# Optimization experiments

Hardware: AMD Instinct MI355X
Metric: run time of the kernel (lower is better)

The kernel has to match this reference:

```python
import jax, jax.numpy as jnp
import numpy as np

N, E = 50000, 800000
DIN, DOUT, DIM, K = 64, 64, 3, 8
EPS_GMM = 1e-15
BN_EPS = 1e-5
ALPHA = 0.01


def setup_inputs() -> dict:
    key = jax.random.key(0)
    ks = jax.random.split(key, 10)
    x = jax.random.normal(ks[0], (N, DIN), dtype=jnp.float32)
    edge_idx = jax.random.randint(ks[1], (2, E), 0, N, dtype=jnp.int64)
    edge_attr = jax.random.uniform(ks[2], (E, DIM), dtype=jnp.float32)
    # GMMConv params (PyG: g maps in -> K*out, lin is root weight, plus bias)
    W_g = jax.random.normal(ks[3], (DIN, K * DOUT), dtype=jnp.float32) * (1.0 / np.sqrt(DIN))
    mu = jax.random.normal(ks[4], (K, DIM), dtype=jnp.float32)
    sigma = jnp.ones((K, DIM), dtype=jnp.float32) + 0.1 * jax.random.normal(ks[5], (K, DIM), dtype=jnp.float32)
    W_root = jax.random.normal(ks[6], (DIN, DOUT), dtype=jnp.float32) * (1.0 / np.sqrt(DIN))
    bias = jnp.zeros((DOUT,), dtype=jnp.float32)
    gamma = jnp.ones((DOUT,), dtype=jnp.float32)
    beta = jnp.zeros((DOUT,), dtype=jnp.float32)
    return {"x": x, "edge_idx": edge_idx, "edge_attr": edge_attr,
            "W_g": W_g, "mu": mu, "sigma": sigma, "W_root": W_root,
            "bias": bias, "gamma": gamma, "beta": beta}


def reference(x, edge_idx, edge_attr, W_g, mu, sigma, W_root, bias, gamma, beta):
    src, dst = edge_idx[0], edge_idx[1]
    # Gaussian mixture edge weights: [E, K]
    diff = edge_attr[:, None, :] - mu[None, :, :]              # [E, K, DIM]
    gauss = jnp.exp((-0.5 * diff * diff / (EPS_GMM + sigma[None] ** 2)).sum(-1))  # [E, K]
    # Transform node features once: [N, K, DOUT]
    x_trans = (x @ W_g).reshape(N, K, DOUT)
    # Per-edge message: weighted sum over kernels of gathered source features
    msg = jnp.einsum('ekm,ek->em', x_trans[src], gauss)        # [E, DOUT]
    # Mean-aggregate to destination nodes
    agg = jax.ops.segment_sum(msg, dst, num_segments=N)        # [N, DOUT]
    cnt = jax.ops.segment_sum(jnp.ones((E,), dtype=x.dtype), dst, num_segments=N)
    agg = agg / jnp.maximum(cnt, 1.0)[:, None]
    # Root weight + bias
    out = agg + x @ W_root + bias
    # BatchNorm1d (training mode: batch stats, biased variance)
    m = out.mean(axis=0)
    v = ((out - m) ** 2).mean(axis=0)
    out = gamma * (out - m) * jax.lax.rsqrt(v + BN_EPS) + beta
    # LeakyReLU
    return jnp.where(out > 0, out, ALPHA * out)
```

## Files before the change

kernel.cpp:

```cpp
#include <hip/hip_runtime.h>
#include <hip/hip_bf16.h>

#define N_NODES 50000
#define N_EDGES 800000

__device__ __forceinline__ void store_val(float* p, float v) { *p = v; }
__device__ __forceinline__ void store_val(__hip_bfloat16* p, float v) { *p = __float2bfloat16(v); }
__device__ __forceinline__ float load_val(const float* p) { return *p; }
__device__ __forceinline__ float load_val(const __hip_bfloat16* p) { return __bfloat162float(*p); }

__global__ void prep_c1_kernel(const float* __restrict__ sigma, float* __restrict__ c1) {
    int i = threadIdx.x;
    if (i < 24) {
        float s = sigma[i];
        c1[i] = -0.5f / (s * s + 1e-15f);
    }
}

template <typename T>
__global__ void gemm_xt_kernel(const float* __restrict__ x, const float* __restrict__ Wg,
                               T* __restrict__ xt) {
    __shared__ float xs[16][64];
    const int tid = threadIdx.x;
    const int row0 = blockIdx.x << 4;
    for (int i = tid; i < 1024; i += 256) xs[i >> 6][i & 63] = x[(size_t)row0 * 64 + i];
    __syncthreads();

    float acc0[16], acc1[16];
#pragma unroll
    for (int r = 0; r < 16; r++) { acc0[r] = 0.f; acc1[r] = 0.f; }

#pragma unroll 4
    for (int i = 0; i < 64; i++) {
        float w0 = Wg[i * 512 + tid];
        float w1 = Wg[i * 512 + tid + 256];
#pragma unroll
        for (int r = 0; r < 16; r++) {
            float xv = xs[r][i];
            acc0[r] = fmaf(xv, w0, acc0[r]);
            acc1[r] = fmaf(xv, w1, acc1[r]);
        }
    }
#pragma unroll
    for (int r = 0; r < 16; r++) {
        size_t o = ((size_t)(row0 + r)) * 512 + tid;
        store_val(&xt[o], acc0[r]);
        store_val(&xt[o + 256], acc1[r]);
    }
}

template <typename T>
__global__ void edge_kernel(const int* __restrict__ eidx, const float* __restrict__ eattr,
                            const float* __restrict__ mu, const float* __restrict__ c1,
                            const T* __restrict__ xt, float* __restrict__ agg,
                            float* __restrict__ cnt) {
    __shared__ float smu[24], sc1[24];
    const int tid = threadIdx.x;
    if (tid < 24) smu[tid] = mu[tid];
    else if (tid < 48) sc1[tid - 24] = c1[tid - 24];
    __syncthreads();

    const int e = (blockIdx.x << 2) + (tid >> 6);
    const int lane = tid & 63;

    const int src = eidx[e];
    const int dst = eidx[N_EDGES + e];

    const float a0 = eattr[e * 3 + 0];
    const float a1 = eattr[e * 3 + 1];
    const float a2 = eattr[e * 3 + 2];

    const int kk = lane & 7;
    const float d0 = a0 - smu[kk * 3 + 0];
    const float d1 = a1 - smu[kk * 3 + 1];
    const float d2 = a2 - smu[kk * 3 + 2];
    const float gv = __expf(fmaf(d0 * d0, sc1[kk * 3 + 0],
                            fmaf(d1 * d1, sc1[kk * 3 + 1],
                                 d2 * d2 * sc1[kk * 3 + 2])));

    const T* xr = xt + (size_t)src * 512 + lane;
    float xv[8];
#pragma unroll
    for (int k = 0; k < 8; k++) xv[k] = load_val(&xr[k * 64]);

    float v = 0.f;
#pragma unroll
    for (int k = 0; k < 8; k++) {
        float gk = __shfl(gv, k, 64);
        v = fmaf(gk, xv[k], v);
    }

    atomicAdd(&agg[(size_t)dst * 64 + lane], v);
    if (lane == 0) atomicAdd(&cnt[dst], 1.0f);
}

__global__ void root_stats_kernel(const float* __restrict__ x, const float* __restrict__ Wr,
                                  const float* __restrict__ bias, const float* __restrict__ agg,
                                  const float* __restrict__ cnt, float* __restrict__ out_pre,
                                  double* __restrict__ colsum, double* __restrict__ colsumsq) {
    __shared__ float wr[4096];
    __shared__ float rs[256], rsq[256];
    for (int i = threadIdx.x; i < 4096; i += 256) wr[i] = Wr[i];
    __syncthreads();

    const int wave = threadIdx.x >> 6;
    const int lane = threadIdx.x & 63;
    const float b = bias[lane];
    const int stride = gridDim.x * 4;

    float s = 0.f, sq = 0.f;
    for (int n = blockIdx.x * 4 + wave; n < N_NODES; n += stride) {
        float xv = x[(size_t)n * 64 + lane];
        float acc = 0.f;
#pragma unroll
        for (int i = 0; i < 64; i++)
            acc = fmaf(__shfl(xv, i, 64), wr[i * 64 + lane], acc);
        float c = cnt[n];
        float val = agg[(size_t)n * 64 + lane] / fmaxf(c, 1.f) + acc + b;
        out_pre[(size_t)n * 64 + lane] = val;
        s += val;
        sq += val * val;
    }

    rs[threadIdx.x] = s;
    rsq[threadIdx.x] = sq;
    __syncthreads();
    if (threadIdx.x < 64) {
        float ts = rs[threadIdx.x] + rs[threadIdx.x + 64] + rs[threadIdx.x + 128] + rs[threadIdx.x + 192];
        float tq = rsq[threadIdx.x] + rsq[threadIdx.x + 64] + rsq[threadIdx.x + 128] + rsq[threadIdx.x + 192];
        atomicAdd(&colsum[threadIdx.x], (double)ts);
        atomicAdd(&colsumsq[threadIdx.x], (double)tq);
    }
}

__global__ void bn_prep_kernel(const double* __restrict__ colsum, const double* __restrict__ colsumsq,
                               float* __restrict__ meanr) {
    int c = threadIdx.x;
    if (c < 64) {
        double m = colsum[c] / (double)N_NODES;
        double var = colsumsq[c] / (double)N_NODES - m * m;
        meanr[c] = (float)m;
        meanr[64 + c] = (float)(1.0 / sqrt(var + 1e-5));
    }
}

__global__ void finalize_kernel(float* __restrict__ out, const float* __restrict__ meanr,
                                const float* __restrict__ gamma, const float* __restrict__ beta) {
    const int i = blockIdx.x * 256 + threadIdx.x;
    const int c = i & 63;
    float v = out[i];
    float o = fmaf((v - meanr[c]) * meanr[64 + c], gamma[c], beta[c]);
    out[i] = o > 0.f ? o : 0.01f * o;
}

extern "C" void kernel_launch(void* const* d_in, const int* in_sizes, int n_in,
                              void* d_out, int out_size, void* d_ws, size_t ws_size,
                              hipStream_t stream) {
    const float* x     = (const float*)d_in[0];
    const int*   eidx  = (const int*)d_in[1];
    const float* eattr = (const float*)d_in[2];
    const float* Wg    = (const float*)d_in[3];
    const float* mu    = (const float*)d_in[4];
    const float* sigma = (const float*)d_in[5];
    const float* Wr    = (const float*)d_in[6];
    const float* bias  = (const float*)d_in[7];
    const float* gamma = (const float*)d_in[8];
    const float* beta  = (const float*)d_in[9];
    float* out = (float*)d_out;

    char* ws = (char*)d_ws;
    const size_t agg_off     = 0;
    const size_t cnt_off     = agg_off + (size_t)N_NODES * 64 * 4;
    const size_t colsum_off  = cnt_off + (size_t)N_NODES * 4;
    const size_t colsumsq_off = colsum_off + 64 * 8;
    const size_t meanr_off   = colsumsq_off + 64 * 8;
    const size_t c1_off      = meanr_off + 128 * 4;
    const size_t xt_off      = c1_off + 128;
    const size_t zero_bytes  = colsumsq_off + 512;

    float*  agg      = (float*)(ws + agg_off);
    float*  cnt      = (float*)(ws + cnt_off);
    double* colsum   = (double*)(ws + colsum_off);
    double* colsumsq = (double*)(ws + colsumsq_off);
    float*  meanr    = (float*)(ws + meanr_off);
    float*  c1       = (float*)(ws + c1_off);

    hipMemsetAsync(ws + agg_off, 0, zero_bytes, stream);
    prep_c1_kernel<<<1, 32, 0, stream>>>(sigma, c1);

    const bool f32path = ws_size >= xt_off + (size_t)N_NODES * 512 * 4;
    if (f32path) {
        float* xt = (float*)(ws + xt_off);
        gemm_xt_kernel<float><<<N_NODES / 16, 256, 0, stream>>>(x, Wg, xt);
        edge_kernel<float><<<N_EDGES / 4, 256, 0, stream>>>(eidx, eattr, mu, c1, xt, agg, cnt);
    } else {
        __hip_bfloat16* xt = (__hip_bfloat16*)(ws + xt_off);
        gemm_xt_kernel<__hip_bfloat16><<<N_NODES / 16, 256, 0, stream>>>(x, Wg, xt);
        edge_kernel<__hip_bfloat16><<<N_EDGES / 4, 256, 0, stream>>>(eidx, eattr, mu, c1, xt, agg, cnt);
    }

    root_stats_kernel<<<1024, 256, 0, stream>>>(x, Wr, bias, agg, cnt, out, colsum, colsumsq);
    bn_prep_kernel<<<1, 64, 0, stream>>>(colsum, colsumsq, meanr);
    finalize_kernel<<<(N_NODES * 64) / 256, 256, 0, stream>>>(out, meanr, gamma, beta);
}
```

Before: 486.8 us.

## Bucket edges by destination and aggregate in shared memory with bf16 features

```diff
diff --git a/kernel.cpp b/kernel.cpp
--- a/kernel.cpp
+++ b/kernel.cpp
@@ -3,142 +3,210 @@
 
 #define N_NODES 50000
 #define N_EDGES 800000
-
-__device__ __forceinline__ void store_val(float* p, float v) { *p = v; }
-__device__ __forceinline__ void store_val(__hip_bfloat16* p, float v) { *p = __float2bfloat16(v); }
-__device__ __forceinline__ float load_val(const float* p) { return *p; }
-__device__ __forceinline__ float load_val(const __hip_bfloat16* p) { return __bfloat162float(*p); }
-
-__global__ void prep_c1_kernel(const float* __restrict__ sigma, float* __restrict__ c1) {
-    int i = threadIdx.x;
-    if (i < 24) {
-        float s = sigma[i];
-        c1[i] = -0.5f / (s * s + 1e-15f);
-    }
-}
-
-template <typename T>
+#define NB 391
+#define BCAP 2560
+
+typedef __hip_bfloat16 bf16;
+
+__device__ __forceinline__ float bf_lo(int u) { union { int i; float f; } c; c.i = (unsigned)u << 16; return c.f; }
+__device__ __forceinline__ float bf_hi(int u) { union { int i; float f; } c; c.i = (unsigned)u & 0xffff0000u; return c.f; }
+__device__ __forceinline__ unsigned short bfbits(float f) {
+    bf16 b = __float2bfloat16(f);
+    union { bf16 b; unsigned short u; } c; c.b = b; return c.u;
+}
+
 __global__ void gemm_xt_kernel(const float* __restrict__ x, const float* __restrict__ Wg,
-                               T* __restrict__ xt) {
+                               bf16* __restrict__ xt) {
     __shared__ float xs[16][64];
+    __shared__ float lb[16 * 512];
     const int tid = threadIdx.x;
     const int row0 = blockIdx.x << 4;
     for (int i = tid; i < 1024; i += 256) xs[i >> 6][i & 63] = x[(size_t)row0 * 64 + i];
     __syncthreads();
 
-    float acc0[16], acc1[16];
-#pragma unroll
-    for (int r = 0; r < 16; r++) { acc0[r] = 0.f; acc1[r] = 0.f; }
-
+    float a0[16], a1[16];
+#pragma unroll
+    for (int r = 0; r < 16; r++) { a0[r] = 0.f; a1[r] = 0.f; }
 #pragma unroll 4
     for (int i = 0; i < 64; i++) {
-        float w0 = Wg[i * 512 + tid];
-        float w1 = Wg[i * 512 + tid + 256];
+        const float w0 = Wg[i * 512 + tid];
+        const float w1 = Wg[i * 512 + tid + 256];
 #pragma unroll
         for (int r = 0; r < 16; r++) {
-            float xv = xs[r][i];
-            acc0[r] = fmaf(xv, w0, acc0[r]);
-            acc1[r] = fmaf(xv, w1, acc1[r]);
+            const float xv = xs[r][i];
+            a0[r] = fmaf(xv, w0, a0[r]);
+            a1[r] = fmaf(xv, w1, a1[r]);
         }
     }
 #pragma unroll
     for (int r = 0; r < 16; r++) {
-        size_t o = ((size_t)(row0 + r)) * 512 + tid;
-        store_val(&xt[o], acc0[r]);
-        store_val(&xt[o + 256], acc1[r]);
-    }
-}
-
-template <typename T>
-__global__ void edge_kernel(const int* __restrict__ eidx, const float* __restrict__ eattr,
-                            const float* __restrict__ mu, const float* __restrict__ c1,
-                            const T* __restrict__ xt, float* __restrict__ agg,
-                            float* __restrict__ cnt) {
+        lb[r * 512 + tid] = a0[r];
+        lb[r * 512 + tid + 256] = a1[r];
+    }
+    __syncthreads();
+
+    const int m = tid & 63, rg = tid >> 6;
+#pragma unroll
+    for (int rr = 0; rr < 4; rr++) {
+        const int r = rg * 4 + rr;
+        unsigned short h[8];
+#pragma unroll
+        for (int k = 0; k < 8; k++) h[k] = bfbits(lb[r * 512 + k * 64 + m]);
+        int4 q;
+        q.x = (int)h[0] | ((int)h[1] << 16);
+        q.y = (int)h[2] | ((int)h[3] << 16);
+        q.z = (int)h[4] | ((int)h[5] << 16);
+        q.w = (int)h[6] | ((int)h[7] << 16);
+        ((int4*)(xt + (size_t)(row0 + r) * 512))[m] = q;
+    }
+}
+
+__global__ void __launch_bounds__(1024) scatter_kernel(const int* __restrict__ eidx,
+                                                       const float* __restrict__ eattr,
+                                                       const float* __restrict__ mu,
+                                                       const float* __restrict__ sigma,
+                                                       int* __restrict__ cursor,
+                                                       unsigned* __restrict__ meta,
+                                                       int4* __restrict__ g8v) {
     __shared__ float smu[24], sc1[24];
+    __shared__ int cnt[NB], base[NB];
     const int tid = threadIdx.x;
-    if (tid < 24) smu[tid] = mu[tid];
-    else if (tid < 48) sc1[tid - 24] = c1[tid - 24];
-    __syncthreads();
-
-    const int e = (blockIdx.x << 2) + (tid >> 6);
-    const int lane = tid & 63;
-
-    const int src = eidx[e];
-    const int dst = eidx[N_EDGES + e];
-
-    const float a0 = eattr[e * 3 + 0];
-    const float a1 = eattr[e * 3 + 1];
-    const float a2 = eattr[e * 3 + 2];
-
-    const int kk = lane & 7;
-    const float d0 = a0 - smu[kk * 3 + 0];
-    const float d1 = a1 - smu[kk * 3 + 1];
-    const float d2 = a2 - smu[kk * 3 + 2];
-    const float gv = __expf(fmaf(d0 * d0, sc1[kk * 3 + 0],
-                            fmaf(d1 * d1, sc1[kk * 3 + 1],
-                                 d2 * d2 * sc1[kk * 3 + 2])));
-
-    const T* xr = xt + (size_t)src * 512 + lane;
-    float xv[8];
-#pragma unroll
-    for (int k = 0; k < 8; k++) xv[k] = load_val(&xr[k * 64]);
-
-    float v = 0.f;
-#pragma unroll
-    for (int k = 0; k < 8; k++) {
-        float gk = __shfl(gv, k, 64);
-        v = fmaf(gk, xv[k], v);
-    }
-
-    atomicAdd(&agg[(size_t)dst * 64 + lane], v);
-    if (lane == 0) atomicAdd(&cnt[dst], 1.0f);
-}
-
-__global__ void root_stats_kernel(const float* __restrict__ x, const float* __restrict__ Wr,
-                                  const float* __restrict__ bias, const float* __restrict__ agg,
-                                  const float* __restrict__ cnt, float* __restrict__ out_pre,
-                                  double* __restrict__ colsum, double* __restrict__ colsumsq) {
+    if (tid < 24) {
+        smu[tid] = mu[tid];
+        const float s = sigma[tid];
+        sc1[tid] = -0.5f / (s * s + 1e-15f);
+    }
+    if (tid < NB) cnt[tid] = 0;
+    __syncthreads();
+
+    const int e = blockIdx.x * 1024 + tid;
+    const bool act = e < N_EDGES;
+    int b = 0, rank = 0;
+    unsigned mt = 0;
+    int4 q = {0, 0, 0, 0};
+    if (act) {
+        const int src = eidx[e];
+        const int dst = eidx[N_EDGES + e];
+        const float A0 = eattr[3 * e + 0];
+        const float A1 = eattr[3 * e + 1];
+        const float A2 = eattr[3 * e + 2];
+        unsigned short h[8];
+#pragma unroll
+        for (int k = 0; k < 8; k++) {
+            const float d0 = A0 - smu[3 * k + 0];
+            const float d1 = A1 - smu[3 * k + 1];
+            const float d2 = A2 - smu[3 * k + 2];
+            const float g = __expf(fmaf(d0 * d0, sc1[3 * k + 0],
+                                   fmaf(d1 * d1, sc1[3 * k + 1],
+                                        d2 * d2 * sc1[3 * k + 2])));
+            h[k] = bfbits(g);
+        }
+        q.x = (int)h[0] | ((int)h[1] << 16);
+        q.y = (int)h[2] | ((int)h[3] << 16);
+        q.z = (int)h[4] | ((int)h[5] << 16);
+        q.w = (int)h[6] | ((int)h[7] << 16);
+        b = dst >> 7;
+        mt = (unsigned)src | ((unsigned)(dst & 127) << 16);
+        rank = atomicAdd(&cnt[b], 1);
+    }
+    __syncthreads();
+    if (tid < NB) {
+        const int c = cnt[tid];
+        base[tid] = c ? atomicAdd(&cursor[tid], c) : 0;
+    }
+    __syncthreads();
+    if (act) {
+        const int slot = b * BCAP + base[b] + rank;
+        meta[slot] = mt;
+        g8v[slot] = q;
+    }
+}
+
+__global__ void __launch_bounds__(1024) agg_kernel(const int* __restrict__ cursor,
+                                                   const unsigned* __restrict__ meta,
+                                                   const int4* __restrict__ g8v,
+                                                   const bf16* __restrict__ xt,
+                                                   const float* __restrict__ x,
+                                                   const float* __restrict__ Wr,
+                                                   const float* __restrict__ bias,
+                                                   float* __restrict__ out,
+                                                   double* __restrict__ colsum,
+                                                   double* __restrict__ colsumsq) {
+    __shared__ float acc[128 * 64];
     __shared__ float wr[4096];
-    __shared__ float rs[256], rsq[256];
-    for (int i = threadIdx.x; i < 4096; i += 256) wr[i] = Wr[i];
-    __syncthreads();
-
-    const int wave = threadIdx.x >> 6;
-    const int lane = threadIdx.x & 63;
-    const float b = bias[lane];
-    const int stride = gridDim.x * 4;
-
+    __shared__ int cnt[128];
+    __shared__ float red[16 * 64];
+
+    const int tid = threadIdx.x;
+    const int b = blockIdx.x;
+    for (int i = tid; i < 8192; i += 1024) acc[i] = 0.f;
+    if (tid < 128) cnt[tid] = 0;
+    for (int i = tid; i < 4096; i += 1024) wr[i] = Wr[i];
+    __syncthreads();
+
+    int count = cursor[b];
+    if (count > BCAP) count = BCAP;
+    const int wid = tid >> 6, lane = tid & 63;
+    const int baseSlot = b * BCAP;
+
+    for (int j = wid; j < count; j += 16) {
+        const unsigned mt = meta[baseSlot + j];
+        const int4 g = g8v[baseSlot + j];
+        const int src = mt & 0xffff;
+        const int dl = (mt >> 16) & 127;
+        const int4 qx = *(const int4*)(xt + (size_t)src * 512 + lane * 8);
+        const float v = bf_lo(g.x) * bf_lo(qx.x) + bf_hi(g.x) * bf_hi(qx.x)
+                      + bf_lo(g.y) * bf_lo(qx.y) + bf_hi(g.y) * bf_hi(qx.y)
+                      + bf_lo(g.z) * bf_lo(qx.z) + bf_hi(g.z) * bf_hi(qx.z)
+                      + bf_lo(g.w) * bf_lo(qx.w) + bf_hi(g.w) * bf_hi(qx.w);
+        atomicAdd(&acc[dl * 64 + lane], v);
+        if (lane == 0) atomicAdd(&cnt[dl], 1);
+    }
+    __syncthreads();
+
+    const float bsv = bias[lane];
     float s = 0.f, sq = 0.f;
-    for (int n = blockIdx.x * 4 + wave; n < N_NODES; n += stride) {
-        float xv = x[(size_t)n * 64 + lane];
-        float acc = 0.f;
-#pragma unroll
-        for (int i = 0; i < 64; i++)
-            acc = fmaf(__shfl(xv, i, 64), wr[i * 64 + lane], acc);
-        float c = cnt[n];
-        float val = agg[(size_t)n * 64 + lane] / fmaxf(c, 1.f) + acc + b;
-        out_pre[(size_t)n * 64 + lane] = val;
-        s += val;
-        sq += val * val;
-    }
-
-    rs[threadIdx.x] = s;
-    rsq[threadIdx.x] = sq;
-    __syncthreads();
-    if (threadIdx.x < 64) {
-        float ts = rs[threadIdx.x] + rs[threadIdx.x + 64] + rs[threadIdx.x + 128] + rs[threadIdx.x + 192];
-        float tq = rsq[threadIdx.x] + rsq[threadIdx.x + 64] + rsq[threadIdx.x + 128] + rsq[threadIdx.x + 192];
-        atomicAdd(&colsum[threadIdx.x], (double)ts);
-        atomicAdd(&colsumsq[threadIdx.x], (double)tq);
+#pragma unroll
+    for (int t = 0; t < 8; t++) {
+        const int nl = wid * 8 + t;
+        const int n = b * 128 + nl;
+        if (n < N_NODES) {
+            const float* xr = x + (size_t)n * 64;
+            float a = 0.f;
+#pragma unroll
+            for (int i = 0; i < 64; i++) a = fmaf(xr[i], wr[i * 64 + lane], a);
+            const float c = (float)cnt[nl];
+            const float val = acc[nl * 64 + lane] / fmaxf(c, 1.f) + a + bsv;
+            out[(size_t)n * 64 + lane] = val;
+            s += val;
+            sq += val * val;
+        }
+    }
+    red[wid * 64 + lane] = s;
+    __syncthreads();
+    float ts = 0.f;
+    if (wid == 0) {
+#pragma unroll
+        for (int w = 0; w < 16; w++) ts += red[w * 64 + lane];
+    }
+    __syncthreads();
+    red[wid * 64 + lane] = sq;
+    __syncthreads();
+    if (wid == 0) {
+        float tq = 0.f;
+#pragma unroll
+        for (int w = 0; w < 16; w++) tq += red[w * 64 + lane];
+        atomicAdd(&colsum[lane], (double)ts);
+        atomicAdd(&colsumsq[lane], (double)tq);
     }
 }
 
 __global__ void bn_prep_kernel(const double* __restrict__ colsum, const double* __restrict__ colsumsq,
                                float* __restrict__ meanr) {
-    int c = threadIdx.x;
+    const int c = threadIdx.x;
     if (c < 64) {
-        double m = colsum[c] / (double)N_NODES;
-        double var = colsumsq[c] / (double)N_NODES - m * m;
+        const double m = colsum[c] / (double)N_NODES;
+        const double var = colsumsq[c] / (double)N_NODES - m * m;
         meanr[c] = (float)m;
         meanr[64 + c] = (float)(1.0 / sqrt(var + 1e-5));
     }
@@ -148,8 +216,8 @@
                                 const float* __restrict__ gamma, const float* __restrict__ beta) {
     const int i = blockIdx.x * 256 + threadIdx.x;
     const int c = i & 63;
-    float v = out[i];
-    float o = fmaf((v - meanr[c]) * meanr[64 + c], gamma[c], beta[c]);
+    const float v = out[i];
+    const float o = fmaf((v - meanr[c]) * meanr[64 + c], gamma[c], beta[c]);
     out[i] = o > 0.f ? o : 0.01f * o;
 }
 
@@ -169,37 +237,27 @@
     float* out = (float*)d_out;
 
     char* ws = (char*)d_ws;
-    const size_t agg_off     = 0;
-    const size_t cnt_off     = agg_off + (size_t)N_NODES * 64 * 4;
-    const size_t colsum_off  = cnt_off + (size_t)N_NODES * 4;
-    const size_t colsumsq_off = colsum_off + 64 * 8;
-    const size_t meanr_off   = colsumsq_off + 64 * 8;
-    const size_t c1_off      = meanr_off + 128 * 4;
-    const size_t xt_off      = c1_off + 128;
-    const size_t zero_bytes  = colsumsq_off + 512;
-
-    float*  agg      = (float*)(ws + agg_off);
-    float*  cnt      = (float*)(ws + cnt_off);
-    double* colsum   = (double*)(ws + colsum_off);
-    double* colsumsq = (double*)(ws + colsumsq_off);
-    float*  meanr    = (float*)(ws + meanr_off);
-    float*  c1       = (float*)(ws + c1_off);
-
-    hipMemsetAsync(ws + agg_off, 0, zero_bytes, stream);
-    prep_c1_kernel<<<1, 32, 0, stream>>>(sigma, c1);
-
-    const bool f32path = ws_size >= xt_off + (size_t)N_NODES * 512 * 4;
-    if (f32path) {
-        float* xt = (float*)(ws + xt_off);
-        gemm_xt_kernel<float><<<N_NODES / 16, 256, 0, stream>>>(x, Wg, xt);
-        edge_kernel<float><<<N_EDGES / 4, 256, 0, stream>>>(eidx, eattr, mu, c1, xt, agg, cnt);
-    } else {
-        __hip_bfloat16* xt = (__hip_bfloat16*)(ws + xt_off);
-        gemm_xt_kernel<__hip_bfloat16><<<N_NODES / 16, 256, 0, stream>>>(x, Wg, xt);
-        edge_kernel<__hip_bfloat16><<<N_EDGES / 4, 256, 0, stream>>>(eidx, eattr, mu, c1, xt, agg, cnt);
-    }
-
-    root_stats_kernel<<<1024, 256, 0, stream>>>(x, Wr, bias, agg, cnt, out, colsum, colsumsq);
+    const size_t cursor_off   = 0;
+    const size_t colsum_off   = 2048;
+    const size_t colsumsq_off = 2560;
+    const size_t zero_bytes   = 3072;
+    const size_t meanr_off    = 3072;
+    const size_t meta_off     = 3584;
+    const size_t g8_off       = 4017664;
+    const size_t xt_off       = 20073984;
+
+    int*      cursor   = (int*)(ws + cursor_off);
+    double*   colsum   = (double*)(ws + colsum_off);
+    double*   colsumsq = (double*)(ws + colsumsq_off);
+    float*    meanr    = (float*)(ws + meanr_off);
+    unsigned* meta     = (unsigned*)(ws + meta_off);
+    int4*     g8v      = (int4*)(ws + g8_off);
+    bf16*     xt       = (bf16*)(ws + xt_off);
+
+    hipMemsetAsync(ws, 0, zero_bytes, stream);
+    gemm_xt_kernel<<<N_NODES / 16, 256, 0, stream>>>(x, Wg, xt);
+    scatter_kernel<<<(N_EDGES + 1023) / 1024, 1024, 0, stream>>>(eidx, eattr, mu, sigma, cursor, meta, g8v);
+    agg_kernel<<<NB, 1024, 0, stream>>>(cursor, meta, g8v, xt, x, Wr, bias, out, colsum, colsumsq);
     bn_prep_kernel<<<1, 64, 0, stream>>>(colsum, colsumsq, meanr);
     finalize_kernel<<<(N_NODES * 64) / 256, 256, 0, stream>>>(out, meanr, gamma, beta);
 }
```

Result: slower. 587.6 us (+20.7%).
